# Optimization experiments

Measured on AMD Instinct MI355X. Metric: run time of the kernel, lower is better.

## Reference

```python
import jax, jax.numpy as jnp
import numpy as np

NEG_SLOPE = 0.01


def reference(feat_src, feat_dst, src, dst, attn_l, attn_r):
    # feat_src: [Ns, D], feat_dst: [Nd, D], src/dst: [E] int, attn_*: [1, D]
    n_dst = feat_dst.shape[0]
    el = (feat_src * attn_l).sum(axis=-1)  # [Ns]
    er = (feat_dst * attn_r).sum(axis=-1)  # [Nd]
    e = el[src] + er[dst]                  # [E]
    e = jnp.where(e >= 0, e, NEG_SLOPE * e)  # leaky_relu
    # edge softmax over incoming edges of each destination node
    m = jax.ops.segment_max(e, dst, num_segments=n_dst)  # [Nd]
    m = jnp.where(jnp.isfinite(m), m, 0.0)  # guard empty segments
    a = jnp.exp(e - m[dst])                 # [E]
    denom = jax.ops.segment_sum(a, dst, num_segments=n_dst)  # [Nd]
    denom = jnp.where(denom > 0, denom, 1.0)
    a = a / denom[dst]
    # weighted scatter-sum of source features: [E, D] messages -> [Nd, D]
    msg = feat_src[src] * a[:, None]
    out = jax.ops.segment_sum(msg, dst, num_segments=n_dst)
    return out


def setup_inputs() -> dict:
    key = jax.random.key(0)
    k1, k2, k3, k4, k5, k6 = jax.random.split(key, 6)
    Ns, Nd, E, D = 100000, 100000, 1600000, 128
    return {
        "feat_src": jax.random.normal(k1, (Ns, D), dtype=jnp.float32),
        "feat_dst": jax.random.normal(k2, (Nd, D), dtype=jnp.float32),
        "src": jax.random.randint(k3, (E,), 0, Ns, dtype=jnp.int32),
        "dst": jax.random.randint(k4, (E,), 0, Nd, dtype=jnp.int32),
        "attn_l": jax.random.normal(k5, (1, D), dtype=jnp.float32) * 0.1,
        "attn_r": jax.random.normal(k6, (1, D), dtype=jnp.float32) * 0.1,
    }
```

## Files before the change

kernel.cpp:

```cpp
#include <hip/hip_runtime.h>
#include <hip/hip_bf16.h>
#include <math.h>

#define D 128
#define AGG_THREADS 128
#define CHUNK 512
#define BSHIFT 6
#define BK 64
#define MAXB 2048
#define MAXWG 1024
#define PCHUNK 4096
#define PE 16
#define EBUF_CAP 1792
#define PR 2048

__device__ __forceinline__ unsigned short f2bf(float f) {
    union { float f; unsigned int u; } c; c.f = f;
    unsigned int u = c.u;
    unsigned int r = (u + 0x7FFFu + ((u >> 16) & 1u)) >> 16;
    return (unsigned short)r;
}
__device__ __forceinline__ void unpack2(unsigned int w, float& lo, float& hi) {
    union { unsigned int u; float f; } c;
    c.u = w << 16;          lo = c.f;
    c.u = w & 0xFFFF0000u;  hi = c.f;
}

__global__ void prep_kernel(const float* __restrict__ feat_src,
                            const float* __restrict__ feat_dst,
                            const float* __restrict__ attn_l,
                            const float* __restrict__ attn_r,
                            float* __restrict__ el, float* __restrict__ er,
                            unsigned short* __restrict__ feat_bf, int store_bf,
                            int Ns, int Nd) {
    int half = threadIdx.x >> 5;
    int lane = threadIdx.x & 31;
    int node = blockIdx.x * 8 + half;
    if (node >= Ns + Nd) return;
    bool is_src = node < Ns;
    const float* feat = is_src ? feat_src + (size_t)node * D
                               : feat_dst + (size_t)(node - Ns) * D;
    const float* attn = is_src ? attn_l : attn_r;
    float4 a = ((const float4*)attn)[lane];
    float4 v = ((const float4*)feat)[lane];
    if (is_src && store_bf) {
        ushort4 h; h.x = f2bf(v.x); h.y = f2bf(v.y); h.z = f2bf(v.z); h.w = f2bf(v.w);
        ((ushort4*)(feat_bf + (size_t)node * D))[lane] = h;
    }
    float s = v.x * a.x + v.y * a.y + v.z * a.z + v.w * a.w;
    #pragma unroll
    for (int off = 16; off > 0; off >>= 1)
        s += __shfl_xor(s, off, 64);
    if (lane == 0) {
        if (is_src) el[node] = s;
        else        er[node - Ns] = s;
    }
}

__global__ void partition_kernel(const int* __restrict__ src, const int* __restrict__ dst,
                                 int E, int nbk,
                                 uint2* __restrict__ bins,
                                 int* __restrict__ cnt_tab, int* __restrict__ loc_tab) {
    __shared__ int hist[MAXB];
    __shared__ int lstart[MAXB];
    __shared__ int cursor[MAXB];
    __shared__ uint2 sbuf[PCHUNK];
    int w = blockIdx.x, tid = threadIdx.x;
    int e0 = w * PCHUNK;
    int e1 = min(E, e0 + PCHUNK);
    int n = e1 - e0;

    for (int i = tid; i < nbk; i += 256) hist[i] = 0;
    __syncthreads();

    int es[PE], ed[PE];
    #pragma unroll
    for (int k = 0; k < PE; ++k) {
        int idx = e0 + k * 256 + tid;
        if (idx < e1) {
            es[k] = src[idx];
            ed[k] = dst[idx];
            atomicAdd(&hist[ed[k] >> BSHIFT], 1);
        }
    }
    __syncthreads();

    if (tid < 64) {
        int carry = 0;
        for (int c = 0; c < nbk; c += 64) {
            int i = c + tid;
            int v = (i < nbk) ? hist[i] : 0;
            int x = v;
            #pragma unroll
            for (int off = 1; off < 64; off <<= 1) {
                int t = __shfl_up(x, off, 64);
                if (tid >= off) x += t;
            }
            if (i < nbk) lstart[i] = x - v + carry;
            carry += __shfl(x, 63, 64);
        }
    }
    __syncthreads();

    for (int i = tid; i < nbk; i += 256) {
        cnt_tab[(size_t)w * nbk + i] = hist[i];
        loc_tab[(size_t)w * nbk + i] = lstart[i];
        cursor[i] = 0;
    }
    __syncthreads();

    #pragma unroll
    for (int k = 0; k < PE; ++k) {
        int idx = e0 + k * 256 + tid;
        if (idx < e1) {
            int b = ed[k] >> BSHIFT;
            int r = lstart[b] + atomicAdd(&cursor[b], 1);
            sbuf[r] = make_uint2((unsigned)es[k], (unsigned)ed[k]);
        }
    }
    __syncthreads();

    uint2* obase = bins + (size_t)w * PCHUNK;
    for (int t = tid; t < n; t += 256) obase[t] = sbuf[t];
}

__global__ void bucket_kernel(const uint2* __restrict__ bins,
                              const int* __restrict__ cnt_tab, const int* __restrict__ loc_tab,
                              int nbk, int nwg,
                              int* __restrict__ counts, int* __restrict__ offs,
                              int* __restrict__ perm, int Nd) {
    __shared__ uint2 ebuf[EBUF_CAP];
    __shared__ int wcnt[MAXWG];
    __shared__ int wdst[MAXWG];
    __shared__ int sbase[MAXWG];
    __shared__ int cntB[BK];
    __shared__ int offB[BK];
    __shared__ int curB[BK];
    __shared__ int total_sh;

    int b = blockIdx.x, tid = threadIdx.x;
    int base = b << BSHIFT;

    for (int i = tid; i < nwg; i += 256) wcnt[i] = cnt_tab[(size_t)i * nbk + b];
    if (tid < BK) { cntB[tid] = 0; curB[tid] = 0; }
    __syncthreads();
    if (tid < 64) {
        int carry = 0;
        for (int c = 0; c < nwg; c += 64) {
            int i = c + tid;
            int v = (i < nwg) ? wcnt[i] : 0;
            int x = v;
            #pragma unroll
            for (int off = 1; off < 64; off <<= 1) {
                int t = __shfl_up(x, off, 64);
                if (tid >= off) x += t;
            }
            if (i < nwg) wdst[i] = x - v + carry;
            carry += __shfl(x, 63, 64);
        }
        if (tid == 0) total_sh = carry;
    }
    __syncthreads();
    int n = total_sh;
    bool fits = (n <= EBUF_CAP);

    if (fits) {
        for (int w = tid; w < nwg; w += 256)
            sbase[w] = w * PCHUNK + loc_tab[(size_t)w * nbk + b] - wdst[w];
        __syncthreads();
        for (int t = tid; t < n; t += 256) {
            int lo = 0, hi = nwg - 1;
            while (lo < hi) {
                int mid = (lo + hi + 1) >> 1;
                if (wdst[mid] <= t) lo = mid; else hi = mid - 1;
            }
            uint2 e = bins[(size_t)(sbase[lo] + t)];
            ebuf[t] = e;
            atomicAdd(&cntB[(int)e.y - base], 1);
        }
    } else {
        for (int w = tid; w < nwg; w += 256) {
            int c = wcnt[w];
            const uint2* sp = bins + (size_t)w * PCHUNK + loc_tab[(size_t)w * nbk + b];
            for (int k = 0; k < c; ++k)
                atomicAdd(&cntB[(int)sp[k].y - base], 1);
        }
    }
    __syncthreads();

    if (tid < 64) {
        int v = cntB[tid];
        int x = v;
        #pragma unroll
        for (int off = 1; off < 64; off <<= 1) {
            int t = __shfl_up(x, off, 64);
            if (tid >= off) x += t;
        }
        int myoff = x - v;
        offB[tid] = myoff;
        int i = base + tid;
        if (i < Nd) {
            int c = v;
            if (myoff + c > PR) c = max(0, PR - myoff);
            counts[i] = c;
            offs[i]   = myoff;
        }
    }
    __syncthreads();

    size_t rbase = (size_t)b * PR;
    if (fits) {
        for (int t = tid; t < n; t += 256) {
            uint2 e = ebuf[t];
            int d = (int)e.y - base;
            int r = atomicAdd(&curB[d], 1);
            int slot = offB[d] + r;
            if (slot < PR) perm[rbase + slot] = (int)e.x;
        }
    } else {
        for (int w = tid; w < nwg; w += 256) {
            int c = wcnt[w];
            const uint2* sp = bins + (size_t)w * PCHUNK + loc_tab[(size_t)w * nbk + b];
            for (int k = 0; k < c; ++k) {
                uint2 e = sp[k];
                int d = (int)e.y - base;
                int r = atomicAdd(&curB[d], 1);
                int slot = offB[d] + r;
                if (slot < PR) perm[rbase + slot] = (int)e.x;
            }
        }
    }
}

__device__ __forceinline__ float block_max128(float v, float* red, int tid) {
    #pragma unroll
    for (int off = 32; off > 0; off >>= 1)
        v = fmaxf(v, __shfl_down(v, off, 64));
    __syncthreads();
    if ((tid & 63) == 0) red[tid >> 6] = v;
    __syncthreads();
    return fmaxf(red[0], red[1]);
}
__device__ __forceinline__ float block_sum128(float v, float* red, int tid) {
    #pragma unroll
    for (int off = 32; off > 0; off >>= 1)
        v += __shfl_down(v, off, 64);
    __syncthreads();
    if ((tid & 63) == 0) red[tid >> 6] = v;
    __syncthreads();
    return red[0] + red[1];
}

__global__ void gat_aggregate_wave_kernel(const unsigned short* __restrict__ feat_bf,
                                          const float* __restrict__ el,
                                          const float* __restrict__ er,
                                          const int* __restrict__ offs,
                                          const int* __restrict__ counts,
                                          const int* __restrict__ perm,
                                          float* __restrict__ out, int Nd) {
    int wid  = threadIdx.x >> 6;
    int lane = threadIdx.x & 63;
    int j = blockIdx.x * 4 + wid;
    if (j >= Nd) return;
    int cnt = counts[j];
    size_t orow = (size_t)j * D;
    if (cnt == 0) {
        ((float2*)(out + orow))[lane] = make_float2(0.0f, 0.0f);
        return;
    }
    size_t beg = (size_t)(j >> BSHIFT) * PR + (size_t)offs[j];
    float erj = er[j];
    int sg = lane >> 4, u = lane & 15;
    const unsigned short* fb = feat_bf + (size_t)u * 8;
    float acc[8];
    #pragma unroll
    for (int k = 0; k < 8; ++k) acc[k] = 0.0f;

    if (cnt <= 64) {
        int s = 0; float e = -INFINITY;
        if (lane < cnt) {
            s = perm[beg + lane];
            float t = el[s] + erj;
            e = (t >= 0.0f) ? t : 0.01f * t;
        }
        float m = e;
        #pragma unroll
        for (int off = 32; off > 0; off >>= 1)
            m = fmaxf(m, __shfl_xor(m, off, 64));
        float a = (lane < cnt) ? __expf(e - m) : 0.0f;
        float den = a;
        #pragma unroll
        for (int off = 32; off > 0; off >>= 1)
            den += __shfl_xor(den, off, 64);
        a *= (1.0f / den);
        int nit = (cnt + 3) >> 2;
        for (int it = 0; it < nit; ++it) {
            int t = sg + (it << 2);
            int tt = (t < cnt) ? t : 0;
            float w = __shfl(a, tt, 64);
            int st  = __shfl(s, tt, 64);
            if (t < cnt) {
                uint4 v = *(const uint4*)(fb + (size_t)st * D);
                float f[8];
                unpack2(v.x, f[0], f[1]); unpack2(v.y, f[2], f[3]);
                unpack2(v.z, f[4], f[5]); unpack2(v.w, f[6], f[7]);
                #pragma unroll
                for (int k = 0; k < 8; ++k) acc[k] += w * f[k];
            }
        }
    } else {
        float lmax = -INFINITY;
        for (int t = lane; t < cnt; t += 64) {
            int s = perm[beg + t];
            float e = el[s] + erj;
            e = (e >= 0.0f) ? e : 0.01f * e;
            lmax = fmaxf(lmax, e);
        }
        float m = lmax;
        #pragma unroll
        for (int off = 32; off > 0; off >>= 1)
            m = fmaxf(m, __shfl_xor(m, off, 64));
        float lsum = 0.0f;
        for (int t = lane; t < cnt; t += 64) {
            int s = perm[beg + t];
            float e = el[s] + erj;
            e = (e >= 0.0f) ? e : 0.01f * e;
            lsum += __expf(e - m);
        }
        #pragma unroll
        for (int off = 32; off > 0; off >>= 1)
            lsum += __shfl_xor(lsum, off, 64);
        float inv = 1.0f / lsum;
        for (int bb = 0; bb < cnt; bb += 64) {
            int nn = min(64, cnt - bb);
            int s = 0; float a = 0.0f;
            if (lane < nn) {
                s = perm[beg + bb + lane];
                float e = el[s] + erj;
                e = (e >= 0.0f) ? e : 0.01f * e;
                a = __expf(e - m) * inv;
            }
            int nit = (nn + 3) >> 2;
            for (int it = 0; it < nit; ++it) {
                int t = sg + (it << 2);
                int tt = (t < nn) ? t : 0;
                float w = __shfl(a, tt, 64);
                int st  = __shfl(s, tt, 64);
                if (t < nn) {
                    uint4 v = *(const uint4*)(fb + (size_t)st * D);
                    float f[8];
                    unpack2(v.x, f[0], f[1]); unpack2(v.y, f[2], f[3]);
                    unpack2(v.z, f[4], f[5]); unpack2(v.w, f[6], f[7]);
                    #pragma unroll
                    for (int k = 0; k < 8; ++k) acc[k] += w * f[k];
                }
            }
        }
    }
    #pragma unroll
    for (int k = 0; k < 8; ++k) {
        acc[k] += __shfl_xor(acc[k], 16, 64);
        acc[k] += __shfl_xor(acc[k], 32, 64);
    }
    if (sg == 0) {
        float* op = out + orow + (size_t)u * 8;
        ((float4*)op)[0] = make_float4(acc[0], acc[1], acc[2], acc[3]);
        ((float4*)op)[1] = make_float4(acc[4], acc[5], acc[6], acc[7]);
    }
}

#define FSHIFT 8
__global__ void hist_kernel(const int* __restrict__ dst, int E, int* __restrict__ counts) {
    int stride = gridDim.x * blockDim.x;
    for (int k = blockIdx.x * blockDim.x + threadIdx.x; k < E; k += stride)
        atomicAdd(&counts[dst[k]], 1);
}
__global__ void scan1_kernel(const int* __restrict__ counts, int* __restrict__ offsets,
                             int* __restrict__ blockSums, int N) {
    __shared__ int tile[256];
    int tid = threadIdx.x;
    int i = blockIdx.x * 256 + tid;
    int v = (i < N) ? counts[i] : 0;
    tile[tid] = v;
    __syncthreads();
    for (int off = 1; off < 256; off <<= 1) {
        int t = (tid >= off) ? tile[tid - off] : 0;
        __syncthreads();
        tile[tid] += t;
        __syncthreads();
    }
    int incl = tile[tid];
    if (i < N) offsets[i] = incl - v;
    if (tid == 255) blockSums[blockIdx.x] = incl;
}
__global__ void scan2_kernel(int* __restrict__ bs, int nb) {
    __shared__ int tile[256];
    int tid = threadIdx.x;
    int carry = 0;
    for (int base = 0; base < nb; base += 256) {
        int i = base + tid;
        int v = (i < nb) ? bs[i] : 0;
        __syncthreads();
        tile[tid] = v;
        __syncthreads();
        for (int off = 1; off < 256; off <<= 1) {
            int t = (tid >= off) ? tile[tid - off] : 0;
            __syncthreads();
            tile[tid] += t;
            __syncthreads();
        }
        int incl = tile[tid];
        if (i < nb) bs[i] = incl - v + carry;
        carry += tile[255];
    }
}
__global__ void fill_kernel(const int* __restrict__ src, const int* __restrict__ dst, int E,
                            const int* __restrict__ offsets, const int* __restrict__ bsum,
                            int* __restrict__ cursor, int* __restrict__ perm_src) {
    int stride = gridDim.x * blockDim.x;
    for (int k = blockIdx.x * blockDim.x + threadIdx.x; k < E; k += stride) {
        int j = dst[k];
        int p = offsets[j] + bsum[j >> FSHIFT] + atomicAdd(&cursor[j], 1);
        perm_src[p] = src[k];
    }
}
__global__ void gat_aggregate_f32_kernel(const float* __restrict__ feat_src,
                                         const float* __restrict__ el,
                                         const float* __restrict__ er,
                                         const int* __restrict__ offsets,
                                         const int* __restrict__ bsum,
                                         const int* __restrict__ counts,
                                         const int* __restrict__ perm_src,
                                         float* __restrict__ out, int Nd) {
    __shared__ float w_sh[CHUNK];
    __shared__ int   s_sh[CHUNK];
    __shared__ float red[2];
    int j = blockIdx.x;
    int tid = threadIdx.x;
    int cnt = counts[j];
    size_t orow = (size_t)j * D;
    if (cnt == 0) { out[orow + tid] = 0.0f; return; }
    int beg = offsets[j] + bsum[j >> FSHIFT];
    float erj = er[j];
    float acc = 0.0f;
    float inv;
    if (cnt <= CHUNK) {
        float lmax = -INFINITY;
        for (int t = tid; t < cnt; t += AGG_THREADS) {
            int s = perm_src[beg + t];
            float e = el[s] + erj;
            e = (e >= 0.0f) ? e : 0.01f * e;
            s_sh[t] = s; w_sh[t] = e;
            lmax = fmaxf(lmax, e);
        }
        float m = block_max128(lmax, red, tid);
        float lsum = 0.0f;
        for (int t = tid; t < cnt; t += AGG_THREADS) {
            float a = __expf(w_sh[t] - m);
            w_sh[t] = a; lsum += a;
        }
        float den = block_sum128(lsum, red, tid);
        inv = 1.0f / den;
        __syncthreads();
        for (int t = 0; t < cnt; ++t)
            acc += feat_src[(size_t)s_sh[t] * D + tid] * w_sh[t];
    } else {
        float lmax = -INFINITY;
        for (int t = tid; t < cnt; t += AGG_THREADS) {
            int s = perm_src[beg + t];
            float e = el[s] + erj;
            e = (e >= 0.0f) ? e : 0.01f * e;
            lmax = fmaxf(lmax, e);
        }
        float m = block_max128(lmax, red, tid);
        float lsum = 0.0f;
        for (int t = tid; t < cnt; t += AGG_THREADS) {
            int s = perm_src[beg + t];
            float e = el[s] + erj;
            e = (e >= 0.0f) ? e : 0.01f * e;
            lsum += __expf(e - m);
        }
        float den = block_sum128(lsum, red, tid);
        inv = 1.0f / den;
        for (int bb = 0; bb < cnt; bb += CHUNK) {
            int n = min(CHUNK, cnt - bb);
            __syncthreads();
            for (int t = tid; t < n; t += AGG_THREADS) {
                int s = perm_src[beg + bb + t];
                float e = el[s] + erj;
                e = (e >= 0.0f) ? e : 0.01f * e;
                s_sh[t] = s;
                w_sh[t] = __expf(e - m);
            }
            __syncthreads();
            for (int t = 0; t < n; ++t)
                acc += feat_src[(size_t)s_sh[t] * D + tid] * w_sh[t];
        }
    }
    out[orow + tid] = acc * inv;
}

extern "C" void kernel_launch(void* const* d_in, const int* in_sizes, int n_in,
                              void* d_out, int out_size, void* d_ws, size_t ws_size,
                              hipStream_t stream) {
    const float* feat_src = (const float*)d_in[0];
    const float* feat_dst = (const float*)d_in[1];
    const int*   src      = (const int*)d_in[2];
    const int*   dst      = (const int*)d_in[3];
    const float* attn_l   = (const float*)d_in[4];
    const float* attn_r   = (const float*)d_in[5];
    float* out = (float*)d_out;

    int Ns = in_sizes[0] / D;
    int Nd = in_sizes[1] / D;
    int E  = in_sizes[2];
    int NBK = (Nd + BK - 1) >> BSHIFT;
    int NFB = (Nd + 255) >> FSHIFT;
    int NWG = (E + PCHUNK - 1) / PCHUNK;

    char* p = (char*)d_ws;
    auto carve = [&](size_t bytes) { void* r = (void*)p; p += (bytes + 255) & ~(size_t)255; return r; };
    float* el      = (float*)carve((size_t)Ns * 4);
    float* er      = (float*)carve((size_t)Nd * 4);
    int*   counts  = (int*)carve((size_t)Nd * 4);
    int*   offs    = (int*)carve((size_t)Nd * 4);
    int*   gcursor = (int*)carve((size_t)Nd * 4);
    int*   bsums   = (int*)carve((size_t)NFB * 4);
    int*   cnt_tab = (int*)carve((size_t)NWG * NBK * 4);
    int*   loc_tab = (int*)carve((size_t)NWG * NBK * 4);
    int*   perm    = (int*)carve((size_t)NBK * PR * 4);
    uint2* bins    = (uint2*)carve((size_t)NWG * PCHUNK * 8);
    size_t used    = (size_t)(p - (char*)d_ws);
    size_t bf_bytes = (size_t)Ns * D * 2;
    unsigned short* feat_bf = (unsigned short*)carve(bf_bytes);

    int fast = (NBK <= MAXB && NWG <= MAXWG &&
                used + bf_bytes + 256 <= ws_size) ? 1 : 0;

    int total = Ns + Nd;
    if (fast) {
        prep_kernel<<<(total + 7) / 8, 256, 0, stream>>>(feat_src, feat_dst, attn_l, attn_r,
                                                         el, er, feat_bf, 1, Ns, Nd);
        partition_kernel<<<NWG, 256, 0, stream>>>(src, dst, E, NBK, bins, cnt_tab, loc_tab);
        bucket_kernel<<<NBK, 256, 0, stream>>>(bins, cnt_tab, loc_tab, NBK, NWG,
                                               counts, offs, perm, Nd);
        gat_aggregate_wave_kernel<<<(Nd + 3) / 4, 256, 0, stream>>>(feat_bf, el, er, offs,
                                                                    counts, perm, out, Nd);
    } else {
        hipMemsetAsync(counts, 0, (size_t)Nd * 4, stream);
        hipMemsetAsync(gcursor, 0, (size_t)Nd * 4, stream);
        prep_kernel<<<(total + 7) / 8, 256, 0, stream>>>(feat_src, feat_dst, attn_l, attn_r,
                                                         el, er, nullptr, 0, Ns, Nd);
        hist_kernel<<<2048, 256, 0, stream>>>(dst, E, counts);
        scan1_kernel<<<NFB, 256, 0, stream>>>(counts, offs, bsums, Nd);
        scan2_kernel<<<1, 256, 0, stream>>>(bsums, NFB);
        fill_kernel<<<2048, 256, 0, stream>>>(src, dst, E, offs, bsums, gcursor, perm);
        gat_aggregate_f32_kernel<<<Nd, AGG_THREADS, 0, stream>>>(feat_src, el, er, offs,
                                                                 bsums, counts, perm, out, Nd);
    }
}
```

Baseline: 270.8 us.

## Halve partition chunk, parallelize scans across four waves, unroll gather loop by two

After: 272.9 us. No clear change (+0.8%).

```diff
diff --git a/kernel.cpp b/kernel.cpp
--- a/kernel.cpp
+++ b/kernel.cpp
@@ -9,8 +9,8 @@
 #define BK 64
 #define MAXB 2048
 #define MAXWG 1024
-#define PCHUNK 4096
-#define PE 16
+#define PCHUNK 2048
+#define PE 8
 #define EBUF_CAP 1792
 #define PR 2048
 
@@ -24,6 +24,38 @@
     union { unsigned int u; float f; } c;
     c.u = w << 16;          lo = c.f;
     c.u = w & 0xFFFF0000u;  hi = c.f;
+}
+
+__device__ __forceinline__ void scan4w(const int* __restrict__ arr, int* __restrict__ outp,
+                                       int n, int tid, int* wsum4) {
+    int wv = tid >> 6, lane = tid & 63;
+    int nchunk = (n + 63) >> 6;
+    int cpw = (nchunk + 3) >> 2;
+    int c0 = wv * cpw, c1 = min(nchunk, c0 + cpw);
+    int carry = 0;
+    for (int c = c0; c < c1; ++c) {
+        int i = (c << 6) + lane;
+        int v = (i < n) ? arr[i] : 0;
+        int x = v;
+        #pragma unroll
+        for (int off = 1; off < 64; off <<= 1) {
+            int t = __shfl_up(x, off, 64);
+            if (lane >= off) x += t;
+        }
+        if (i < n) outp[i] = x - v + carry;
+        carry += __shfl(x, 63, 64);
+    }
+    if (lane == 0) wsum4[wv] = carry;
+    __syncthreads();
+    int wbase = 0;
+    for (int u = 0; u < wv; ++u) wbase += wsum4[u];
+    if (wbase) {
+        for (int c = c0; c < c1; ++c) {
+            int i = (c << 6) + lane;
+            if (i < n) outp[i] += wbase;
+        }
+    }
+    __syncthreads();
 }
 
 __global__ void prep_kernel(const float* __restrict__ feat_src,
@@ -65,6 +97,7 @@
     __shared__ int lstart[MAXB];
     __shared__ int cursor[MAXB];
     __shared__ uint2 sbuf[PCHUNK];
+    __shared__ int wsum4[4];
     int w = blockIdx.x, tid = threadIdx.x;
     int e0 = w * PCHUNK;
     int e1 = min(E, e0 + PCHUNK);
@@ -85,22 +118,7 @@
     }
     __syncthreads();
 
-    if (tid < 64) {
-        int carry = 0;
-        for (int c = 0; c < nbk; c += 64) {
-            int i = c + tid;
-            int v = (i < nbk) ? hist[i] : 0;
-            int x = v;
-            #pragma unroll
-            for (int off = 1; off < 64; off <<= 1) {
-                int t = __shfl_up(x, off, 64);
-                if (tid >= off) x += t;
-            }
-            if (i < nbk) lstart[i] = x - v + carry;
-            carry += __shfl(x, 63, 64);
-        }
-    }
-    __syncthreads();
+    scan4w(hist, lstart, nbk, tid, wsum4);
 
     for (int i = tid; i < nbk; i += 256) {
         cnt_tab[(size_t)w * nbk + i] = hist[i];
@@ -136,7 +154,7 @@
     __shared__ int cntB[BK];
     __shared__ int offB[BK];
     __shared__ int curB[BK];
-    __shared__ int total_sh;
+    __shared__ int wsum4[4];
 
     int b = blockIdx.x, tid = threadIdx.x;
     int base = b << BSHIFT;
@@ -144,24 +162,9 @@
     for (int i = tid; i < nwg; i += 256) wcnt[i] = cnt_tab[(size_t)i * nbk + b];
     if (tid < BK) { cntB[tid] = 0; curB[tid] = 0; }
     __syncthreads();
-    if (tid < 64) {
-        int carry = 0;
-        for (int c = 0; c < nwg; c += 64) {
-            int i = c + tid;
-            int v = (i < nwg) ? wcnt[i] : 0;
-            int x = v;
-            #pragma unroll
-            for (int off = 1; off < 64; off <<= 1) {
-                int t = __shfl_up(x, off, 64);
-                if (tid >= off) x += t;
-            }
-            if (i < nwg) wdst[i] = x - v + carry;
-            carry += __shfl(x, 63, 64);
-        }
-        if (tid == 0) total_sh = carry;
-    }
-    __syncthreads();
-    int n = total_sh;
+
+    scan4w(wcnt, wdst, nwg, tid, wsum4);
+    int n = wsum4[0] + wsum4[1] + wsum4[2] + wsum4[3];
     bool fits = (n <= EBUF_CAP);
 
     if (fits) {
@@ -294,18 +297,42 @@
             den += __shfl_xor(den, off, 64);
         a *= (1.0f / den);
         int nit = (cnt + 3) >> 2;
-        for (int it = 0; it < nit; ++it) {
-            int t = sg + (it << 2);
-            int tt = (t < cnt) ? t : 0;
-            float w = __shfl(a, tt, 64);
-            int st  = __shfl(s, tt, 64);
-            if (t < cnt) {
-                uint4 v = *(const uint4*)(fb + (size_t)st * D);
+        int it = 0;
+        for (; it + 2 <= nit; it += 2) {
+            int t0 = sg + (it << 2);
+            int t1 = t0 + 4;
+            int u1 = (t1 < cnt) ? t1 : 0;
+            float w0 = __shfl(a, t0, 64);
+            int   s0 = __shfl(s, t0, 64);
+            float w1 = __shfl(a, u1, 64);
+            int   s1 = __shfl(s, u1, 64);
+            bool p1 = (t1 < cnt);
+            uint4 v0 = *(const uint4*)(fb + (size_t)s0 * D);
+            uint4 v1 = p1 ? *(const uint4*)(fb + (size_t)s1 * D) : make_uint4(0,0,0,0);
+            float f[8];
+            unpack2(v0.x, f[0], f[1]); unpack2(v0.y, f[2], f[3]);
+            unpack2(v0.z, f[4], f[5]); unpack2(v0.w, f[6], f[7]);
+            #pragma unroll
+            for (int k = 0; k < 8; ++k) acc[k] += w0 * f[k];
+            if (p1) {
+                unpack2(v1.x, f[0], f[1]); unpack2(v1.y, f[2], f[3]);
+                unpack2(v1.z, f[4], f[5]); unpack2(v1.w, f[6], f[7]);
+                #pragma unroll
+                for (int k = 0; k < 8; ++k) acc[k] += w1 * f[k];
+            }
+        }
+        if (it < nit) {
+            int t0 = sg + (it << 2);
+            int u0 = (t0 < cnt) ? t0 : 0;
+            float w0 = __shfl(a, u0, 64);
+            int   s0 = __shfl(s, u0, 64);
+            if (t0 < cnt) {
+                uint4 v0 = *(const uint4*)(fb + (size_t)s0 * D);
                 float f[8];
-                unpack2(v.x, f[0], f[1]); unpack2(v.y, f[2], f[3]);
-                unpack2(v.z, f[4], f[5]); unpack2(v.w, f[6], f[7]);
+                unpack2(v0.x, f[0], f[1]); unpack2(v0.y, f[2], f[3]);
+                unpack2(v0.z, f[4], f[5]); unpack2(v0.w, f[6], f[7]);
                 #pragma unroll
-                for (int k = 0; k < 8; ++k) acc[k] += w * f[k];
+                for (int k = 0; k < 8; ++k) acc[k] += w0 * f[k];
             }
         }
     } else {
```
